# Kernel tuning notes

Measured on AMD Instinct MI355X. Metric: run time of the kernel, lower is better.

## Reference

```python
import jax, jax.numpy as jnp
import numpy as np

N = 8192  # n_nodes
E = 262144  # edges per adjacency (avg degree 32)


def setup_inputs() -> dict:
    key = jax.random.key(0)
    k0, k1, k2, k3, k4, k5 = jax.random.split(key, 6)
    rows_s = jax.random.randint(k0, (E,), 0, N)
    cols_s = jax.random.randint(k1, (E,), 0, N)
    vals_s = jax.random.uniform(k2, (E,), dtype=jnp.float32)
    rows_t = jax.random.randint(k3, (E,), 0, N)
    cols_t = jax.random.randint(k4, (E,), 0, N)
    vals_t = jax.random.uniform(k5, (E,), dtype=jnp.float32)
    gamma = jnp.zeros((1,), dtype=jnp.float32)  # learnable scalar, init 0.0
    return {
        "rows_s": rows_s, "cols_s": cols_s, "vals_s": vals_s,
        "rows_t": rows_t, "cols_t": cols_t, "vals_t": vals_t,
        "gamma": gamma,
    }


def reference(rows_s, cols_s, vals_s, rows_t, cols_t, vals_t, gamma):
    # coalesce + to_dense: scatter-add duplicates into dense [N, N]
    As = jnp.zeros((N, N), dtype=vals_s.dtype).at[rows_s, cols_s].add(vals_s)
    At = jnp.zeros((N, N), dtype=vals_t.dtype).at[rows_t, cols_t].add(vals_t)
    alpha = jax.nn.sigmoid(gamma[0])
    Af = alpha * As + (1.0 - alpha) * At
    row_sum = jnp.sum(Af, axis=1, keepdims=True)  # [N, 1]
    row_sum = jnp.where(row_sum == 0, jnp.ones_like(row_sum), row_sum)
    Af = Af / row_sum
    # torch returns Af.to_sparse(); dense Af is the equivalent value-complete output
    return Af
```

## Files before the change

kernel.cpp:

```cpp
#include <hip/hip_runtime.h>
#include <math.h>

#define NN 8192
#define NE 262144
#define TOTAL (2*NE)
#define CAP 128

typedef float f4 __attribute__((ext_vector_type(4)));

struct Pair { int c; float v; };

#define BK_OFF (65536)
#define OV_OFF (65536 + (size_t)NN * CAP * 8)

__global__ __launch_bounds__(256) void fill_kernel(
        const int* __restrict__ rows_s, const int* __restrict__ cols_s,
        const float* __restrict__ vals_s,
        const int* __restrict__ rows_t, const int* __restrict__ cols_t,
        const float* __restrict__ vals_t,
        const float* __restrict__ gamma,
        int* __restrict__ cnt, Pair* __restrict__ bucket,
        int* __restrict__ ovf_cnt, int4* __restrict__ ovf) {
    int i = blockIdx.x * blockDim.x + threadIdx.x;
    float alpha = 1.0f / (1.0f + expf(-gamma[0]));
    int r, c; float v, w;
    if (i < NE) { r = rows_s[i]; c = cols_s[i]; v = vals_s[i]; w = alpha; }
    else { int j = i - NE; r = rows_t[j]; c = cols_t[j]; v = vals_t[j]; w = 1.0f - alpha; }
    float wv = w * v;
    int pos = atomicAdd(&cnt[r], 1);
    if (pos < CAP) {
        Pair p; p.c = c; p.v = wv;
        bucket[r * CAP + pos] = p;
    } else {
        int k = atomicAdd(ovf_cnt, 1);
        int4 e; e.x = r; e.y = c; e.z = __float_as_int(wv); e.w = 0;
        ovf[k] = e;
    }
}

__global__ __launch_bounds__(256) void row_kernel(
        const int* __restrict__ cnt, const Pair* __restrict__ bucket,
        const int* __restrict__ ovf_cnt, const int4* __restrict__ ovf,
        float* __restrict__ out) {
    __shared__ float row[NN];
    __shared__ float red[4];
    int r = blockIdx.x;
    int t = threadIdx.x;

    f4* row4 = (f4*)row;
    #pragma unroll
    for (int k = t; k < NN / 4; k += 256) {
        f4 z = {0.f, 0.f, 0.f, 0.f};
        row4[k] = z;
    }
    int n = cnt[r];
    int nb = n < CAP ? n : CAP;
    __syncthreads();

    float part = 0.0f;
    for (int k = t; k < nb; k += 256) {
        Pair p = bucket[r * CAP + k];
        part += p.v;
        atomicAdd(&row[p.c], p.v);
    }
    int no = *ovf_cnt;
    if (no > 0) {
        for (int k = t; k < no; k += 256) {
            int4 e = ovf[k];
            if (e.x == r) {
                float v = __int_as_float(e.z);
                part += v;
                atomicAdd(&row[e.y], v);
            }
        }
    }

    #pragma unroll
    for (int o = 32; o > 0; o >>= 1) part += __shfl_down(part, o, 64);
    if ((t & 63) == 0) red[t >> 6] = part;
    __syncthreads();
    float total = red[0] + red[1] + red[2] + red[3];
    float inv = (total == 0.0f) ? 1.0f : 1.0f / total;

    f4* out4 = (f4*)(out + (size_t)r * NN);
    #pragma unroll
    for (int k = t; k < NN / 4; k += 256) {
        f4 x = row4[k];
        x *= inv;
        __builtin_nontemporal_store(x, &out4[k]);
    }
}

extern "C" void kernel_launch(void* const* d_in, const int* in_sizes, int n_in,
                              void* d_out, int out_size, void* d_ws, size_t ws_size,
                              hipStream_t stream) {
    const int*   rows_s = (const int*)  d_in[0];
    const int*   cols_s = (const int*)  d_in[1];
    const float* vals_s = (const float*)d_in[2];
    const int*   rows_t = (const int*)  d_in[3];
    const int*   cols_t = (const int*)  d_in[4];
    const float* vals_t = (const float*)d_in[5];
    const float* gamma  = (const float*)d_in[6];

    float* out     = (float*)d_out;
    char*  ws      = (char*)d_ws;
    int*   cnt     = (int*)ws;
    int*   ovf_cnt = (int*)(ws + 32768);
    Pair*  bucket  = (Pair*)(ws + BK_OFF);
    int4*  ovf     = (int4*)(ws + OV_OFF);

    (void)hipMemsetAsync(ws, 0, 32772, stream);

    fill_kernel<<<TOTAL / 256, 256, 0, stream>>>(rows_s, cols_s, vals_s,
                                                 rows_t, cols_t, vals_t,
                                                 gamma, cnt, bucket, ovf_cnt, ovf);
    row_kernel<<<NN, 256, 0, stream>>>(cnt, bucket, ovf_cnt, ovf, out);
}
```

Before: 308.9 us.

## Fuse memset, fill and row kernels into one cooperative persistent kernel

```diff
diff --git a/kernel.cpp b/kernel.cpp
--- a/kernel.cpp
+++ b/kernel.cpp
@@ -1,10 +1,15 @@
 #include <hip/hip_runtime.h>
+#include <hip/hip_cooperative_groups.h>
 #include <math.h>
+
+namespace cg = cooperative_groups;
 
 #define NN 8192
 #define NE 262144
 #define TOTAL (2*NE)
 #define CAP 128
+#define GRID 1024
+#define NTHREADS (GRID*256)
 
 typedef float f4 __attribute__((ext_vector_type(4)));
 
@@ -13,16 +18,14 @@
 #define BK_OFF (65536)
 #define OV_OFF (65536 + (size_t)NN * CAP * 8)
 
-__global__ __launch_bounds__(256) void fill_kernel(
+__device__ __forceinline__ void fill_one(
+        int i, float alpha,
         const int* __restrict__ rows_s, const int* __restrict__ cols_s,
         const float* __restrict__ vals_s,
         const int* __restrict__ rows_t, const int* __restrict__ cols_t,
         const float* __restrict__ vals_t,
-        const float* __restrict__ gamma,
         int* __restrict__ cnt, Pair* __restrict__ bucket,
         int* __restrict__ ovf_cnt, int4* __restrict__ ovf) {
-    int i = blockIdx.x * blockDim.x + threadIdx.x;
-    float alpha = 1.0f / (1.0f + expf(-gamma[0]));
     int r, c; float v, w;
     if (i < NE) { r = rows_s[i]; c = cols_s[i]; v = vals_s[i]; w = alpha; }
     else { int j = i - NE; r = rows_t[j]; c = cols_t[j]; v = vals_t[j]; w = 1.0f - alpha; }
@@ -38,21 +41,12 @@
     }
 }
 
-__global__ __launch_bounds__(256) void row_kernel(
+__device__ __forceinline__ void do_row(
+        int r, int t, float* row, f4* row4, float* red,
         const int* __restrict__ cnt, const Pair* __restrict__ bucket,
-        const int* __restrict__ ovf_cnt, const int4* __restrict__ ovf,
-        float* __restrict__ out) {
-    __shared__ float row[NN];
-    __shared__ float red[4];
-    int r = blockIdx.x;
-    int t = threadIdx.x;
-
-    f4* row4 = (f4*)row;
+        int no, const int4* __restrict__ ovf, float* __restrict__ out) {
     #pragma unroll
-    for (int k = t; k < NN / 4; k += 256) {
-        f4 z = {0.f, 0.f, 0.f, 0.f};
-        row4[k] = z;
-    }
+    for (int k = t; k < NN / 4; k += 256) { f4 z = {0.f, 0.f, 0.f, 0.f}; row4[k] = z; }
     int n = cnt[r];
     int nb = n < CAP ? n : CAP;
     __syncthreads();
@@ -63,7 +57,6 @@
         part += p.v;
         atomicAdd(&row[p.c], p.v);
     }
-    int no = *ovf_cnt;
     if (no > 0) {
         for (int k = t; k < no; k += 256) {
             int4 e = ovf[k];
@@ -74,7 +67,6 @@
             }
         }
     }
-
     #pragma unroll
     for (int o = 32; o > 0; o >>= 1) part += __shfl_down(part, o, 64);
     if ((t & 63) == 0) red[t >> 6] = part;
@@ -89,6 +81,64 @@
         x *= inv;
         __builtin_nontemporal_store(x, &out4[k]);
     }
+}
+
+__global__ __launch_bounds__(256) void fused_kernel(
+        const int* __restrict__ rows_s, const int* __restrict__ cols_s,
+        const float* __restrict__ vals_s,
+        const int* __restrict__ rows_t, const int* __restrict__ cols_t,
+        const float* __restrict__ vals_t,
+        const float* __restrict__ gamma,
+        int* __restrict__ cnt, Pair* __restrict__ bucket,
+        int* __restrict__ ovf_cnt, int4* __restrict__ ovf,
+        float* __restrict__ out) {
+    cg::grid_group grid = cg::this_grid();
+    int tid = blockIdx.x * 256 + threadIdx.x;
+
+    if (tid < NN) cnt[tid] = 0;
+    if (tid == 0) *ovf_cnt = 0;
+    grid.sync();
+
+    float alpha = 1.0f / (1.0f + expf(-gamma[0]));
+    #pragma unroll
+    for (int base = 0; base < TOTAL; base += NTHREADS)
+        fill_one(base + tid, alpha, rows_s, cols_s, vals_s, rows_t, cols_t, vals_t,
+                 cnt, bucket, ovf_cnt, ovf);
+    grid.sync();
+
+    __shared__ float row[NN];
+    __shared__ float red[4];
+    f4* row4 = (f4*)row;
+    int t = threadIdx.x;
+    int no = *ovf_cnt;
+    for (int r = blockIdx.x; r < NN; r += GRID) {
+        do_row(r, t, row, row4, red, cnt, bucket, no, ovf, out);
+        __syncthreads();
+    }
+}
+
+__global__ __launch_bounds__(256) void fill_kernel(
+        const int* __restrict__ rows_s, const int* __restrict__ cols_s,
+        const float* __restrict__ vals_s,
+        const int* __restrict__ rows_t, const int* __restrict__ cols_t,
+        const float* __restrict__ vals_t,
+        const float* __restrict__ gamma,
+        int* __restrict__ cnt, Pair* __restrict__ bucket,
+        int* __restrict__ ovf_cnt, int4* __restrict__ ovf) {
+    int i = blockIdx.x * blockDim.x + threadIdx.x;
+    float alpha = 1.0f / (1.0f + expf(-gamma[0]));
+    fill_one(i, alpha, rows_s, cols_s, vals_s, rows_t, cols_t, vals_t,
+             cnt, bucket, ovf_cnt, ovf);
+}
+
+__global__ __launch_bounds__(256) void row_kernel(
+        const int* __restrict__ cnt, const Pair* __restrict__ bucket,
+        const int* __restrict__ ovf_cnt, const int4* __restrict__ ovf,
+        float* __restrict__ out) {
+    __shared__ float row[NN];
+    __shared__ float red[4];
+    f4* row4 = (f4*)row;
+    do_row(blockIdx.x, threadIdx.x, row, row4, red, cnt, bucket, *ovf_cnt, ovf, out);
 }
 
 extern "C" void kernel_launch(void* const* d_in, const int* in_sizes, int n_in,
@@ -109,10 +159,18 @@
     Pair*  bucket  = (Pair*)(ws + BK_OFF);
     int4*  ovf     = (int4*)(ws + OV_OFF);
 
-    (void)hipMemsetAsync(ws, 0, 32772, stream);
-
-    fill_kernel<<<TOTAL / 256, 256, 0, stream>>>(rows_s, cols_s, vals_s,
-                                                 rows_t, cols_t, vals_t,
-                                                 gamma, cnt, bucket, ovf_cnt, ovf);
-    row_kernel<<<NN, 256, 0, stream>>>(cnt, bucket, ovf_cnt, ovf, out);
+    void* args[] = { (void*)&rows_s, (void*)&cols_s, (void*)&vals_s,
+                     (void*)&rows_t, (void*)&cols_t, (void*)&vals_t,
+                     (void*)&gamma,  (void*)&cnt,    (void*)&bucket,
+                     (void*)&ovf_cnt,(void*)&ovf,    (void*)&out };
+    hipError_t err = hipLaunchCooperativeKernel((const void*)fused_kernel,
+                                                dim3(GRID), dim3(256),
+                                                args, 0, stream);
+    if (err != hipSuccess) {
+        (void)hipMemsetAsync(ws, 0, 32772, stream);
+        fill_kernel<<<TOTAL / 256, 256, 0, stream>>>(rows_s, cols_s, vals_s,
+                                                     rows_t, cols_t, vals_t,
+                                                     gamma, cnt, bucket, ovf_cnt, ovf);
+        row_kernel<<<NN, 256, 0, stream>>>(cnt, bucket, ovf_cnt, ovf, out);
+    }
 }
```

New measurement: 483.9 us. 1.57x slower.
